# Optimization experiments

Measured on AMD Instinct MI355X. Metric: run time of the kernel, lower is better.

The kernel has to match this reference:

```python
import jax, jax.numpy as jnp
import numpy as np

POOLSCALE = 4  # HSA: avg-pool kernel/stride = (scale, scale*4)

def _avg_pool(x, kh, kw):
    # kernel == stride and dims divisible -> exact reshape-mean pooling
    B, C, H, W = x.shape
    return x.reshape(B, C, H // kh, kh, W // kw, kw).mean(axis=(3, 5))

def setup_inputs() -> dict:
    key = jax.random.key(0)
    k1, k2, k3 = jax.random.split(key, 3)
    shape = (4, 64, 192, 192)
    return {
        "K": jax.random.normal(k1, shape, dtype=jnp.float32),
        "Q": jax.random.normal(k2, shape, dtype=jnp.float32),
        "V": jax.random.normal(k3, shape, dtype=jnp.float32),
    }

def reference(K, Q, V):
    B, C, H, W = Q.shape
    kh, kw = POOLSCALE, POOLSCALE * 4
    Qp = Q.reshape(B, C, H * W).transpose(0, 2, 1)          # [B, HW, C]
    Kp = _avg_pool(K, kh, kw)                               # [B, C, h, w]
    Kp = Kp.reshape(B, C, -1)                               # [B, C, hw_p]
    Vp = _avg_pool(V, kh, kw).reshape(B, C, -1)             # [B, C, hw_p]
    scores = jnp.einsum('bnc,bcm->bnm', Qp, Kp)             # [B, HW, hw_p]
    attn = jax.nn.softmax(scores, axis=1)                   # softmax over query dim (dim=1), as in torch code
    out = jnp.einsum('bcm,bnm->bcn', Vp, attn)              # V_pie @ attn^T -> [B, C, HW]
    return out.reshape(B, C, H, W)
```

## Files before the change

kernel.cpp:

```cpp
#include <hip/hip_runtime.h>
#include <stdint.h>

#define BB 4
#define CC 64
#define HH 192
#define WW 192
#define HWN (HH*WW)
#define KH 4
#define KW 16
#define PW (WW/KW)
#define MP ((HH/KH)*(WW/KW))
#define MITER (MP/64)
#define NBTOT (HWN/32)
#define NUNIT (HWN/64)
#define NGRP 36
#define SCALE_W 65536.0f
#define INV_SCALE (1.0f/65536.0f)
#define LOG2E 1.44269504088896f

typedef _Float16 half8 __attribute__((ext_vector_type(8)));
typedef float floatx4 __attribute__((ext_vector_type(4)));

static __device__ __forceinline__ void gload16(const void* g, void* l) {
  __builtin_amdgcn_global_load_lds((const __attribute__((address_space(1))) void*)g,
                                   (__attribute__((address_space(3))) void*)l, 16, 0, 0);
}
#define WAITCNT_VM(N) asm volatile("s_waitcnt vmcnt(" #N ")" ::: "memory")

static __device__ __forceinline__ float fexp2(float x) {
#if __has_builtin(__builtin_amdgcn_exp2f)
  return __builtin_amdgcn_exp2f(x);
#else
  return __expf(x * 0.6931471805599453f);
#endif
}


__global__ __launch_bounds__(256) void pool_kernel(
    const float* __restrict__ Kin, const float* __restrict__ Vin,
    _Float16* __restrict__ kptF, float* __restrict__ vp) {
  int t = blockIdx.x * 256 + threadIdx.x;
  const int total = BB * CC * MP;
  bool isV = t >= total;
  int idx = isV ? t - total : t;
  int m = idx % MP;
  int c = (idx / MP) % CC;
  int b = idx / (MP * CC);
  int mh = m / PW, mw = m % PW;
  const float* src = (isV ? Vin : Kin) + (((b * CC + c) * HH + mh * KH) * WW + mw * KW);
  float s = 0.f;
#pragma unroll
  for (int r = 0; r < KH; ++r) {
    const float4* row = (const float4*)(src + r * WW);
#pragma unroll
    for (int j = 0; j < KW / 4; ++j) {
      float4 v = row[j];
      s += v.x + v.y + v.z + v.w;
    }
  }
  s *= (1.0f / (KH * KW));
  if (isV) {
    vp[(b * CC + c) * MP + m] = s;
  } else {
    int mi = m >> 6, w = m & 63, mf = w >> 4, l15 = w & 15;
    int ks = c >> 5, lhi = (c >> 3) & 3, e = c & 7;
    int lane = lhi * 16 + l15;
    kptF[((((b * MITER + mi) * 4 + mf) * 2 + ks) * 64 + lane) * 8 + e] =
        (_Float16)(s * LOG2E);
  }
}

__global__ __launch_bounds__(256) void qprep_kernel(
    const float* __restrict__ Q, _Float16* __restrict__ qF) {
  int t = blockIdx.x * 256 + threadIdx.x;
  int chunk = t >> 6;
  int lane = t & 63;
  int nf = chunk & 1;
  int ks = (chunk >> 1) & 1;
  int idx = chunk >> 2;
  int nb = idx % NBTOT;
  int b = idx / NBTOT;
  int c0 = ks * 32 + (lane >> 4) * 8;
  int n = nb * 32 + nf * 16 + (lane & 15);
  const float* Qb = Q + (b * CC + c0) * HWN + n;
  half8 h;
#pragma unroll
  for (int e = 0; e < 8; ++e) h[e] = (_Float16)Qb[e * HWN];
  *(half8*)(qF + chunk * 512 + lane * 8) = h;
}

__global__ __launch_bounds__(256) void colsum_qf2_kernel(
    const _Float16* __restrict__ qF, const _Float16* __restrict__ kptF,
    float* __restrict__ part) {
  int tid = threadIdx.x;
  int lane = tid & 63;
  int l15 = lane & 15;
  int u = blockIdx.x * 4 + (tid >> 6);
  int b = u / NUNIT;
  int un = u % NUNIT;

  const _Float16* qc = qF + (size_t)((b * NBTOT + un * 2) * 4) * 512 + lane * 8;
  half8 af[2][2][2];
#pragma unroll
  for (int nb = 0; nb < 2; ++nb)
#pragma unroll
    for (int ks = 0; ks < 2; ++ks)
#pragma unroll
      for (int nf = 0; nf < 2; ++nf)
        af[nb][nf][ks] = *(const half8*)(qc + (nb * 4 + ks * 2 + nf) * 512);

  const _Float16* kb = kptF + b * MITER * 8 * 512;
  floatx4 zero = {0.f, 0.f, 0.f, 0.f};
  float* pout = part + (size_t)(b * NUNIT + un) * MP;

#pragma unroll
  for (int mi = 0; mi < MITER; ++mi) {
    half8 bfr[4][2];
#pragma unroll
    for (int mf = 0; mf < 4; ++mf)
#pragma unroll
      for (int ks = 0; ks < 2; ++ks)
        bfr[mf][ks] = *(const half8*)(kb + ((mi * 4 + mf) * 2 + ks) * 512 + lane * 8);

    float s0 = 0.f, s1 = 0.f, s2 = 0.f, s3 = 0.f;
#pragma unroll
    for (int nb = 0; nb < 2; ++nb) {
      floatx4 sacc[2][4];
#pragma unroll
      for (int nf = 0; nf < 2; ++nf)
#pragma unroll
        for (int mf = 0; mf < 4; ++mf) sacc[nf][mf] = zero;
      __builtin_amdgcn_s_setprio(1);
#pragma unroll
      for (int ks = 0; ks < 2; ++ks)
#pragma unroll
        for (int nf = 0; nf < 2; ++nf)
#pragma unroll
          for (int mf = 0; mf < 4; ++mf)
            sacc[nf][mf] = __builtin_amdgcn_mfma_f32_16x16x32_f16(
                af[nb][nf][ks], bfr[mf][ks], sacc[nf][mf], 0, 0, 0);
      __builtin_amdgcn_s_setprio(0);
#pragma unroll
      for (int nf = 0; nf < 2; ++nf)
#pragma unroll
        for (int r = 0; r < 4; ++r) {
          s0 += fexp2(sacc[nf][0][r]);
          s1 += fexp2(sacc[nf][1][r]);
          s2 += fexp2(sacc[nf][2][r]);
          s3 += fexp2(sacc[nf][3][r]);
        }
    }
    s0 += __shfl_xor(s0, 16); s0 += __shfl_xor(s0, 32);
    s1 += __shfl_xor(s1, 16); s1 += __shfl_xor(s1, 32);
    s2 += __shfl_xor(s2, 16); s2 += __shfl_xor(s2, 32);
    s3 += __shfl_xor(s3, 16); s3 += __shfl_xor(s3, 32);
    if (lane < 16) {
      float* p = pout + mi * 64;
      p[0 * 16 + l15] = s0;
      p[1 * 16 + l15] = s1;
      p[2 * 16 + l15] = s2;
      p[3 * 16 + l15] = s3;
    }
  }
}

__global__ __launch_bounds__(576) void colsum_reduceA_kernel(
    const float* __restrict__ part, float* __restrict__ part2) {
  int m = threadIdx.x;
  int g = blockIdx.x;
  int b = blockIdx.y;
  const float* p = part + (size_t)(b * NUNIT + g * 16) * MP + m;
  float a0 = 0.f, a1 = 0.f, a2 = 0.f, a3 = 0.f;
#pragma unroll
  for (int j = 0; j < 16; j += 4) {
    a0 += p[(size_t)(j + 0) * MP];
    a1 += p[(size_t)(j + 1) * MP];
    a2 += p[(size_t)(j + 2) * MP];
    a3 += p[(size_t)(j + 3) * MP];
  }
  part2[(size_t)(b * NGRP + g) * MP + m] = (a0 + a1) + (a2 + a3);
}

__global__ __launch_bounds__(256) void colsum_reduceB_kernel(
    const float* __restrict__ part2, float* __restrict__ colsum) {
  int t = blockIdx.x * 256 + threadIdx.x;
  int m = t % MP;
  int b = t / MP;
  const float* p = part2 + (size_t)b * NGRP * MP + m;
  float a0 = 0.f, a1 = 0.f, a2 = 0.f, a3 = 0.f;
#pragma unroll
  for (int g = 0; g < NGRP; g += 4) {
    a0 += p[(size_t)(g + 0) * MP];
    a1 += p[(size_t)(g + 1) * MP];
    a2 += p[(size_t)(g + 2) * MP];
    a3 += p[(size_t)(g + 3) * MP];
  }
  colsum[t] = (a0 + a1) + (a2 + a3);
}

__global__ __launch_bounds__(256) void wprep_kernel(
    const float* __restrict__ vp, const float* __restrict__ colsum,
    _Float16* __restrict__ wqF) {
  int t = blockIdx.x * 256 + threadIdx.x;
  int m = t % MP;
  int c = (t / MP) % CC;
  int b = t / (CC * MP);
  float w = vp[t] / colsum[b * MP + m] * SCALE_W;
  int cf = c >> 4, l15 = c & 15;
  int mi = m >> 6, wl = m & 63;
  int ks = wl >> 5, v = wl & 31;
  int lhi = (v & 15) >> 2;
  int e = (v >> 4) * 4 + (v & 3);
  int lane = lhi * 16 + l15;
  wqF[((((b * MITER + mi) * 4 + cf) * 2 + ks) * 64 + lane) * 8 + e] = (_Float16)w;
}

__global__ __launch_bounds__(256) void attn_v4_kernel(
    const _Float16* __restrict__ qF, const _Float16* __restrict__ kptF,
    const _Float16* __restrict__ wqF, float* __restrict__ out) {
  __shared__ char stg[2 * 16384];
  int b = blockIdx.y;
  int tid = threadIdx.x;
  int wv = tid >> 6;
  int lane = tid & 63;
  int l15 = lane & 15, lhi = lane >> 4;

  const _Float16* kb = kptF + b * MITER * 8 * 512;
  const _Float16* wb = wqF + b * MITER * 8 * 512;

#define STAGE_V4(tt, ss)                                                       \
  {                                                                            \
    int q0_ = wv * 4;                                                          \
    _Pragma("unroll") for (int j_ = 0; j_ < 4; ++j_) {                         \
      int q_ = q0_ + j_;                                                       \
      const _Float16* sp_ = (q_ < 8 ? kb + (tt) * 4096 + q_ * 512              \
                                    : wb + (tt) * 4096 + (q_ - 8) * 512) +     \
                            lane * 8;                                          \
      gload16(sp_, stg + (ss) * 16384 + q_ * 1024);                            \
    }                                                                          \
  }

  STAGE_V4(0, 0);

  int nb0 = blockIdx.x * 8 + wv * 2;
  const _Float16* qc = qF + (size_t)((b * NBTOT + nb0) * 4) * 512 + lane * 8;
  half8 afrag[2][2][2];
#pragma unroll
  for (int j = 0; j < 2; ++j)
#pragma unroll
    for (int ks = 0; ks < 2; ++ks)
#pragma unroll
      for (int nf = 0; nf < 2; ++nf)
        afrag[j][nf][ks] = *(const half8*)(qc + (j * 4 + ks * 2 + nf) * 512);

  floatx4 zero = {0.f, 0.f, 0.f, 0.f};
  floatx4 oacc[2][4][2];
#pragma unroll
  for (int j = 0; j < 2; ++j)
#pragma unroll
    for (int cf = 0; cf < 4; ++cf)
#pragma unroll
      for (int nf = 0; nf < 2; ++nf) oacc[j][cf][nf] = zero;

#pragma unroll
  for (int mi = 0; mi < MITER; ++mi) {
    const int sc = mi & 1;
    WAITCNT_VM(0);
    __builtin_amdgcn_sched_barrier(0);
    __builtin_amdgcn_s_barrier();
    if (mi + 1 < MITER) STAGE_V4(mi + 1, sc ^ 1);

    half8 bfr[4][2];
#pragma unroll
    for (int mf = 0; mf < 4; ++mf)
#pragma unroll
      for (int ks = 0; ks < 2; ++ks)
        bfr[mf][ks] = *(const half8*)(stg + sc * 16384 + (mf * 2 + ks) * 1024 + lane * 16);
    half8 wfr[4][2];
#pragma unroll
    for (int cf = 0; cf < 4; ++cf)
#pragma unroll
      for (int ks = 0; ks < 2; ++ks)
        wfr[cf][ks] = *(const half8*)(stg + sc * 16384 + 8192 + (cf * 2 + ks) * 1024 + lane * 16);

#pragma unroll
    for (int j = 0; j < 2; ++j) {
      floatx4 sacc[4][2];
#pragma unroll
      for (int mf = 0; mf < 4; ++mf)
#pragma unroll
        for (int nf = 0; nf < 2; ++nf) sacc[mf][nf] = zero;
      __builtin_amdgcn_s_setprio(1);
#pragma unroll
      for (int ks = 0; ks < 2; ++ks)
#pragma unroll
        for (int mf = 0; mf < 4; ++mf)
#pragma unroll
          for (int nf = 0; nf < 2; ++nf)
            sacc[mf][nf] = __builtin_amdgcn_mfma_f32_16x16x32_f16(
                bfr[mf][ks], afrag[j][nf][ks], sacc[mf][nf], 0, 0, 0);
      __builtin_amdgcn_s_setprio(0);

#pragma unroll
      for (int ks = 0; ks < 2; ++ks) {
        half8 ef[2];
#pragma unroll
        for (int nf = 0; nf < 2; ++nf)
#pragma unroll
          for (int e = 0; e < 8; ++e)
            ef[nf][e] = (_Float16)fexp2(sacc[2 * ks + (e >> 2)][nf][e & 3]);
        __builtin_amdgcn_s_setprio(1);
#pragma unroll
        for (int cf = 0; cf < 4; ++cf)
#pragma unroll
          for (int nf = 0; nf < 2; ++nf)
            oacc[j][cf][nf] = __builtin_amdgcn_mfma_f32_16x16x32_f16(
                wfr[cf][ks], ef[nf], oacc[j][cf][nf], 0, 0, 0);
        __builtin_amdgcn_s_setprio(0);
      }
    }
  }

  float* ob = out + b * CC * HWN;
#pragma unroll
  for (int j = 0; j < 2; ++j)
#pragma unroll
    for (int cf = 0; cf < 4; ++cf)
#pragma unroll
      for (int nf = 0; nf < 2; ++nf)
#pragma unroll
        for (int r = 0; r < 4; ++r) {
          int c = cf * 16 + lhi * 4 + r;
          int n = (nb0 + j) * 32 + nf * 16 + l15;
          ob[c * HWN + n] = oacc[j][cf][nf][r] * INV_SCALE;
        }
}

extern "C" void kernel_launch(void* const* d_in, const int* in_sizes, int n_in,
                              void* d_out, int out_size, void* d_ws, size_t ws_size,
                              hipStream_t stream) {
  const float* K = (const float*)d_in[0];
  const float* Q = (const float*)d_in[1];
  const float* V = (const float*)d_in[2];
  float* out = (float*)d_out;
  char* ws = (char*)d_ws;
  _Float16* kptF  = (_Float16*)(ws);
  float*    vp    = (float*)(ws + 294912);
  _Float16* wqF   = (_Float16*)(ws + 294912 + 589824);
  float*    colsum = (float*)(ws + 294912 + 589824 + 294912);
  const size_t QF_OFF = 1204224;
  _Float16* qF = (_Float16*)(ws + QF_OFF);
  float* part  = out;
  float* part2 = out + 2097152;

  pool_kernel<<<(2 * BB * CC * MP) / 256, 256, 0, stream>>>(K, V, kptF, vp);
  qprep_kernel<<<(BB * NBTOT * 4 * 64) / 256, 256, 0, stream>>>(Q, qF);
  colsum_qf2_kernel<<<(BB * NUNIT) / 4, 256, 0, stream>>>(qF, kptF, part);
  colsum_reduceA_kernel<<<dim3(NGRP, BB), 576, 0, stream>>>(part, part2);
  colsum_reduceB_kernel<<<(BB * MP) / 256, 256, 0, stream>>>(part2, colsum);
  wprep_kernel<<<(BB * CC * MP) / 256, 256, 0, stream>>>(vp, colsum, wqF);
  attn_v4_kernel<<<dim3(NBTOT / 8, BB), 256, 0, stream>>>(qF, kptF, wqF, out);
}
```

Baseline: 84.73 us.

## Merge pooling and Q prep kernels; triple-buffer K/W staging in attention

Combines the K/V pooling kernel and the Q fp16 repack kernel into one launch that branches on block index, removing one kernel launch and letting the two memory-bound passes run concurrently. The attention kernel moves from double to triple-buffered LDS staging. It prefetches two tiles ahead and waits only for the older loads (vmcnt 4), so global-to-LDS copies overlap more with MFMA compute. This raises LDS use per block to 48KB, which may reduce occupancy. The Q fragment loads are also issued before the first stages, so the partial vmcnt wait has to account for them correctly.

```diff
diff --git a/kernel.cpp b/kernel.cpp
--- a/kernel.cpp
+++ b/kernel.cpp
@@ -36,57 +36,59 @@
 }
 
 
-__global__ __launch_bounds__(256) void pool_kernel(
+__global__ __launch_bounds__(256) void prep_kernel(
     const float* __restrict__ Kin, const float* __restrict__ Vin,
-    _Float16* __restrict__ kptF, float* __restrict__ vp) {
-  int t = blockIdx.x * 256 + threadIdx.x;
-  const int total = BB * CC * MP;
-  bool isV = t >= total;
-  int idx = isV ? t - total : t;
-  int m = idx % MP;
-  int c = (idx / MP) % CC;
-  int b = idx / (MP * CC);
-  int mh = m / PW, mw = m % PW;
-  const float* src = (isV ? Vin : Kin) + (((b * CC + c) * HH + mh * KH) * WW + mw * KW);
-  float s = 0.f;
-#pragma unroll
-  for (int r = 0; r < KH; ++r) {
-    const float4* row = (const float4*)(src + r * WW);
-#pragma unroll
-    for (int j = 0; j < KW / 4; ++j) {
-      float4 v = row[j];
-      s += v.x + v.y + v.z + v.w;
-    }
-  }
-  s *= (1.0f / (KH * KW));
-  if (isV) {
-    vp[(b * CC + c) * MP + m] = s;
+    const float* __restrict__ Q,
+    _Float16* __restrict__ kptF, float* __restrict__ vp,
+    _Float16* __restrict__ qF) {
+  const int POOL_BLOCKS = (2 * BB * CC * MP) / 256;
+  if (blockIdx.x < POOL_BLOCKS) {
+    int t = blockIdx.x * 256 + threadIdx.x;
+    const int total = BB * CC * MP;
+    bool isV = t >= total;
+    int idx = isV ? t - total : t;
+    int m = idx % MP;
+    int c = (idx / MP) % CC;
+    int b = idx / (MP * CC);
+    int mh = m / PW, mw = m % PW;
+    const float* src = (isV ? Vin : Kin) + (((b * CC + c) * HH + mh * KH) * WW + mw * KW);
+    float s = 0.f;
+#pragma unroll
+    for (int r = 0; r < KH; ++r) {
+      const float4* row = (const float4*)(src + r * WW);
+#pragma unroll
+      for (int j = 0; j < KW / 4; ++j) {
+        float4 v = row[j];
+        s += v.x + v.y + v.z + v.w;
+      }
+    }
+    s *= (1.0f / (KH * KW));
+    if (isV) {
+      vp[(b * CC + c) * MP + m] = s;
+    } else {
+      int mi = m >> 6, w = m & 63, mf = w >> 4, l15 = w & 15;
+      int ks = c >> 5, lhi = (c >> 3) & 3, e = c & 7;
+      int lane = lhi * 16 + l15;
+      kptF[((((b * MITER + mi) * 4 + mf) * 2 + ks) * 64 + lane) * 8 + e] =
+          (_Float16)(s * LOG2E);
+    }
   } else {
-    int mi = m >> 6, w = m & 63, mf = w >> 4, l15 = w & 15;
-    int ks = c >> 5, lhi = (c >> 3) & 3, e = c & 7;
-    int lane = lhi * 16 + l15;
-    kptF[((((b * MITER + mi) * 4 + mf) * 2 + ks) * 64 + lane) * 8 + e] =
-        (_Float16)(s * LOG2E);
-  }
-}
-
-__global__ __launch_bounds__(256) void qprep_kernel(
-    const float* __restrict__ Q, _Float16* __restrict__ qF) {
-  int t = blockIdx.x * 256 + threadIdx.x;
-  int chunk = t >> 6;
-  int lane = t & 63;
-  int nf = chunk & 1;
-  int ks = (chunk >> 1) & 1;
-  int idx = chunk >> 2;
-  int nb = idx % NBTOT;
-  int b = idx / NBTOT;
-  int c0 = ks * 32 + (lane >> 4) * 8;
-  int n = nb * 32 + nf * 16 + (lane & 15);
-  const float* Qb = Q + (b * CC + c0) * HWN + n;
-  half8 h;
-#pragma unroll
-  for (int e = 0; e < 8; ++e) h[e] = (_Float16)Qb[e * HWN];
-  *(half8*)(qF + chunk * 512 + lane * 8) = h;
+    int t = (blockIdx.x - POOL_BLOCKS) * 256 + threadIdx.x;
+    int chunk = t >> 6;
+    int lane = t & 63;
+    int nf = chunk & 1;
+    int ks = (chunk >> 1) & 1;
+    int idx = chunk >> 2;
+    int nb = idx % NBTOT;
+    int b = idx / NBTOT;
+    int c0 = ks * 32 + (lane >> 4) * 8;
+    int n = nb * 32 + nf * 16 + (lane & 15);
+    const float* Qb = Q + (b * CC + c0) * HWN + n;
+    half8 h;
+#pragma unroll
+    for (int e = 0; e < 8; ++e) h[e] = (_Float16)Qb[e * HWN];
+    *(half8*)(qF + chunk * 512 + lane * 8) = h;
+  }
 }
 
 __global__ __launch_bounds__(256) void colsum_qf2_kernel(
@@ -215,10 +217,10 @@
   wqF[((((b * MITER + mi) * 4 + cf) * 2 + ks) * 64 + lane) * 8 + e] = (_Float16)w;
 }
 
-__global__ __launch_bounds__(256) void attn_v4_kernel(
+__global__ __launch_bounds__(256) void attn_v5_kernel(
     const _Float16* __restrict__ qF, const _Float16* __restrict__ kptF,
     const _Float16* __restrict__ wqF, float* __restrict__ out) {
-  __shared__ char stg[2 * 16384];
+  __shared__ char stg[3 * 16384];
   int b = blockIdx.y;
   int tid = threadIdx.x;
   int wv = tid >> 6;
@@ -228,7 +230,7 @@
   const _Float16* kb = kptF + b * MITER * 8 * 512;
   const _Float16* wb = wqF + b * MITER * 8 * 512;
 
-#define STAGE_V4(tt, ss)                                                       \
+#define STAGE_V5(tt, ss)                                                       \
   {                                                                            \
     int q0_ = wv * 4;                                                          \
     _Pragma("unroll") for (int j_ = 0; j_ < 4; ++j_) {                         \
@@ -240,8 +242,6 @@
     }                                                                          \
   }
 
-  STAGE_V4(0, 0);
-
   int nb0 = blockIdx.x * 8 + wv * 2;
   const _Float16* qc = qF + (size_t)((b * NBTOT + nb0) * 4) * 512 + lane * 8;
   half8 afrag[2][2][2];
@@ -252,6 +252,8 @@
 #pragma unroll
       for (int nf = 0; nf < 2; ++nf)
         afrag[j][nf][ks] = *(const half8*)(qc + (j * 4 + ks * 2 + nf) * 512);
+  STAGE_V5(0, 0);
+  STAGE_V5(1, 1);
 
   floatx4 zero = {0.f, 0.f, 0.f, 0.f};
   floatx4 oacc[2][4][2];
@@ -264,11 +266,11 @@
 
 #pragma unroll
   for (int mi = 0; mi < MITER; ++mi) {
-    const int sc = mi & 1;
-    WAITCNT_VM(0);
+    const int sc = mi % 3;
+    if (mi < MITER - 1) { WAITCNT_VM(4); } else { WAITCNT_VM(0); }
     __builtin_amdgcn_sched_barrier(0);
     __builtin_amdgcn_s_barrier();
-    if (mi + 1 < MITER) STAGE_V4(mi + 1, sc ^ 1);
+    if (mi + 2 < MITER) STAGE_V5(mi + 2, (mi + 2) % 3);
 
     half8 bfr[4][2];
 #pragma unroll
@@ -353,11 +355,12 @@
   float* part  = out;
   float* part2 = out + 2097152;
 
-  pool_kernel<<<(2 * BB * CC * MP) / 256, 256, 0, stream>>>(K, V, kptF, vp);
-  qprep_kernel<<<(BB * NBTOT * 4 * 64) / 256, 256, 0, stream>>>(Q, qF);
+  const int POOL_BLOCKS = (2 * BB * CC * MP) / 256;
+  const int QPREP_BLOCKS = (BB * NBTOT * 4 * 64) / 256;
+  prep_kernel<<<POOL_BLOCKS + QPREP_BLOCKS, 256, 0, stream>>>(K, V, Q, kptF, vp, qF);
   colsum_qf2_kernel<<<(BB * NUNIT) / 4, 256, 0, stream>>>(qF, kptF, part);
   colsum_reduceA_kernel<<<dim3(NGRP, BB), 576, 0, stream>>>(part, part2);
   colsum_reduceB_kernel<<<(BB * MP) / 256, 256, 0, stream>>>(part2, colsum);
   wprep_kernel<<<(BB * CC * MP) / 256, 256, 0, stream>>>(vp, colsum, wqF);
-  attn_v4_kernel<<<dim3(NBTOT / 8, BB), 256, 0, stream>>>(qF, kptF, wqF, out);
-}
+  attn_v5_kernel<<<dim3(NBTOT / 8, BB), 256, 0, stream>>>(qF, kptF, wqF, out);
+}
```

New measurement: 82.42 us. 1.03x faster.
